# Optimization experiments

Measured on AMD Instinct MI355X. Metric: run time of the kernel, lower is better.

## Reference

```python
import jax, jax.numpy as jnp
import numpy as np
from jax import lax

N_GROUPS = 128
EPS = 1e-5


def _instance_norm(x):
    # x: [B, C, H, W]; per-sample per-channel normalization over spatial dims
    mean = jnp.mean(x, axis=(2, 3), keepdims=True)
    var = jnp.mean(jnp.square(x - mean), axis=(2, 3), keepdims=True)
    return (x - mean) * lax.rsqrt(var + EPS)


def _reflect_pad(x, p):
    return jnp.pad(x, ((0, 0), (0, 0), (p, p), (p, p)), mode='reflect')


def _conv(x, w, groups):
    # x: [N, Cin, H, W], w: [Cout, Cin/groups, kh, kw], VALID padding
    return lax.conv_general_dilated(
        x, w, window_strides=(1, 1), padding='VALID',
        dimension_numbers=('NCHW', 'OIHW', 'NCHW'),
        feature_group_count=groups)


def _forward_single(xi, ws, wp, b):
    # xi: [1, C, H, W]; ws: [C_mid, C/G, k, k]; wp: [C_pw, C_mid/G, 1, 1]; b: [C_pw]
    k = ws.shape[-1]
    p = (k - 1) // 2  # k=3 -> ceil/floor both 1
    y = _conv(_reflect_pad(xi, p), ws, N_GROUPS)
    y = _conv(y, wp, N_GROUPS) + b[None, :, None, None]
    return y


def setup_inputs() -> dict:
    key = jax.random.key(0)
    ks = jax.random.split(key, 6)
    B, C, H, W = 4, 512, 128, 128
    x = jax.random.normal(ks[0], (B, C, H, W), dtype=jnp.float32)
    w_spatial = jax.random.normal(ks[1], (B, 512, 4, 3, 3), dtype=jnp.float32) * 0.05
    w_pointwise = jax.random.normal(ks[2], (B, 128, 4, 1, 1), dtype=jnp.float32) * 0.05
    bias = jax.random.normal(ks[3], (B, 128), dtype=jnp.float32) * 0.05
    conv_w = jax.random.normal(ks[4], (512, 512, 3, 3), dtype=jnp.float32) * 0.02
    conv_b = jax.random.normal(ks[5], (512,), dtype=jnp.float32) * 0.02
    return {"x": x, "w_spatial": w_spatial, "w_pointwise": w_pointwise,
            "bias": bias, "conv_w": conv_w, "conv_b": conv_b}


def reference(x, w_spatial, w_pointwise, bias, conv_w, conv_b):
    B, C, H, W = x.shape
    x = _instance_norm(x)
    # per-sample grouped spatial + pointwise conv, vmapped over batch
    ys = jax.vmap(_forward_single)(x[:, None], w_spatial, w_pointwise, bias)
    # ys: [B, 1, C_pw, H, W] -> concat along channel dim as in torch.cat(dim=1)
    ys = ys.reshape(1, B * ys.shape[2], H, W)
    # final standard conv, reflect padding (1,1), kernel 3
    out = _conv(_reflect_pad(ys, 1), conv_w, 1) + conv_b[None, :, None, None]
    return out
```

## Files before the change

### kernel.cpp

```cpp
#include <hip/hip_runtime.h>
#include <hip/hip_bf16.h>


typedef unsigned short u16;
typedef __attribute__((ext_vector_type(8))) short bf16x8;
typedef __attribute__((ext_vector_type(4))) float f32x4;

#define HW 16384
#define NBC 2048

__device__ __forceinline__ int refl(int i) {
    return i < 0 ? -i : (i > 127 ? 254 - i : i);
}

__device__ __forceinline__ u16 f2bf(float f) {
    union { float f; unsigned u; } x; x.f = f;
    unsigned r = x.u + 0x7fffu + ((x.u >> 16) & 1u);
    return (u16)(r >> 16);
}

__device__ __forceinline__ void load_lds16(const u16* g, u16* l) {
    __builtin_amdgcn_global_load_lds(
        (const __attribute__((address_space(1))) unsigned int*)g,
        (__attribute__((address_space(3))) unsigned int*)l, 16, 0, 0);
}

__device__ __forceinline__ void load_lds16f(const float* g, float* l) {
    __builtin_amdgcn_global_load_lds(
        (const __attribute__((address_space(1))) unsigned int*)g,
        (__attribute__((address_space(3))) unsigned int*)l, 16, 0, 0);
}

__device__ __forceinline__ void load_lds4(const float* g, float* l) {
    __builtin_amdgcn_global_load_lds(
        (const __attribute__((address_space(1))) unsigned int*)g,
        (__attribute__((address_space(3))) unsigned int*)l, 4, 0, 0);
}

__global__ __launch_bounds__(256) void stats_kernel(
        const float* __restrict__ x, float* __restrict__ mean,
        float* __restrict__ rstd) {
    int bc = blockIdx.x;
    const float4* p4 = (const float4*)(x + (size_t)bc * HW);
    float s = 0.f, ss = 0.f;
    for (int i = threadIdx.x; i < HW / 4; i += 256) {
        float4 v = p4[i];
        s  += v.x + v.y + v.z + v.w;
        ss += v.x * v.x + v.y * v.y + v.z * v.z + v.w * v.w;
    }
    for (int o = 32; o >= 1; o >>= 1) {
        s  += __shfl_down(s, o);
        ss += __shfl_down(ss, o);
    }
    __shared__ float sm[4], sm2[4];
    int wid = threadIdx.x >> 6, lane = threadIdx.x & 63;
    if (lane == 0) { sm[wid] = s; sm2[wid] = ss; }
    __syncthreads();
    if (threadIdx.x == 0) {
        float S = sm[0] + sm[1] + sm[2] + sm[3];
        float SS = sm2[0] + sm2[1] + sm2[2] + sm2[3];
        float m = S * (1.f / HW);
        float var = SS * (1.f / HW) - m * m;
        mean[bc] = m;
        rstd[bc] = rsqrtf(var + 1e-5f);
    }
}

__global__ __launch_bounds__(256) void weff_kernel(
        const float* __restrict__ wsp, const float* __restrict__ wpw,
        const float* __restrict__ rstd, float* __restrict__ wf) {
    int idx = blockIdx.x * 256 + threadIdx.x;
    if (idx >= 4 * 128 * 4 * 9) return;
    int k = idx % 9;
    int c = (idx / 9) & 3;
    int g = (idx / 36) & 127;
    int b = idx / 4608;
    float acc = 0.f;
#pragma unroll
    for (int m = 0; m < 4; ++m) {
        acc += wpw[(b * 128 + g) * 4 + m] *
               wsp[(((size_t)b * 512 + g * 4 + m) * 4 + c) * 9 + k];
    }
    wf[idx] = acc * rstd[(b << 9) + (g << 2) + c];
}

__global__ __launch_bounds__(256) void bias_fold(
        const float* __restrict__ wf, const float* __restrict__ bias,
        const float* __restrict__ mean, float* __restrict__ bf) {
    int bg = blockIdx.x * 256 + threadIdx.x;
    if (bg >= 512) return;
    float s = bias[bg];
    const float* w = wf + bg * 36;
    const float* m = mean + (bg << 2);
#pragma unroll
    for (int j = 0; j < 36; ++j) s -= w[j] * m[j / 9];
    bf[bg] = s;
}

__global__ __launch_bounds__(256) void wpack_kernel(
        const float* __restrict__ cw, u16* __restrict__ wT) {
    __shared__ float s[4608];
    int t = threadIdx.x, co = blockIdx.x;
    const float* src = cw + (size_t)co * 4608;
    for (int i = t; i < 4608; i += 256) s[i] = src[i];
    __syncthreads();
#pragma unroll
    for (int tap = 0; tap < 9; ++tap) {
        u16* dst = &wT[((size_t)(tap << 9) + co) * 512];
        dst[t]       = f2bf(s[t * 9 + tap]);
        dst[t + 256] = f2bf(s[(t + 256) * 9 + tap]);
    }
}

__global__ __launch_bounds__(512) void midconv_fused(
        const float* __restrict__ x, const float* __restrict__ wf,
        const float* __restrict__ bf, u16* __restrict__ ysT) {
    __shared__ float mid[2][2560];
    __shared__ float halo[2][320];
    __shared__ u16 outb[128 * 72];
    __shared__ float s_w[4608];
    __shared__ float s_b[128];
    int t = threadIdx.x;
    int b = blockIdx.y;
    int x0 = (blockIdx.x & 7) << 4, y0 = (blockIdx.x >> 3) << 3;

    for (int i = t; i < 4608; i += 512) s_w[i] = wf[b * 4608 + i];
    if (t < 128) s_b[t] = bf[(b << 7) + t];

    int smid0, smid1, shalo;
    {
        int ch = t / 40, rem = t - ch * 40;
        int r = rem >> 2, j = rem & 3;
        smid0 = (ch << 14) + (refl(y0 + r - 1) << 7) + x0 + (j << 2);
        int i1 = t + 512 < 640 ? t + 512 : 0;
        ch = i1 / 40; rem = i1 - ch * 40; r = rem >> 2; j = rem & 3;
        smid1 = (ch << 14) + (refl(y0 + r - 1) << 7) + x0 + (j << 2);
        int ih = t < 320 ? t : 0;
        int side = ih >= 160;
        int hh = side ? ih - 160 : ih;
        ch = hh / 10; r = hh - ch * 10;
        int col = side ? refl(x0 + 16) : refl(x0 - 1);
        shalo = (ch << 14) + (refl(y0 + r - 1) << 7) + col;
    }

    int gq = t >> 7;
    int rem = t & 127;
    int py = rem >> 4, px = rem & 15;

    {
        const float* xq = x + ((size_t)(b << 9) << 14);
        load_lds16f(xq + smid0, &mid[0][t * 4]);
        if (t < 128) load_lds16f(xq + smid1, &mid[0][(512 + t) * 4]);
        if (t < 320) load_lds4(xq + shalo, &halo[0][t]);
    }

    for (int q = 0; q < 32; ++q) {
        __syncthreads();
        if (q == 16) {
            for (int i = t; i < 1024; i += 512) {
                int pix = i >> 3, seg = i & 7;
                bf16x8 v = *(const bf16x8*)&outb[pix * 72 + (seg << 3)];
                int ppy = pix >> 4, ppx = pix & 15;
                size_t gp = (size_t)(((y0 + ppy) << 7) + x0 + ppx);
                *(bf16x8*)&ysT[gp * 512 + (b << 7) + (seg << 3)] = v;
            }
            __syncthreads();
        }
        int cur = q & 1;
        if (q < 31) {
            const float* xq = x + ((size_t)((b << 9) + ((q + 1) << 4)) << 14);
            load_lds16f(xq + smid0, &mid[cur ^ 1][t * 4]);
            if (t < 128) load_lds16f(xq + smid1, &mid[cur ^ 1][(512 + t) * 4]);
            if (t < 320) load_lds4(xq + shalo, &halo[cur ^ 1][t]);
        }
        int group = (q << 2) + gq;
        float acc = s_b[group];
        const float* wq = &s_w[group * 36];
#pragma unroll
        for (int c = 0; c < 4; ++c) {
            const float* tp  = &mid[cur][(gq * 4 + c) * 160];
            const float* hlc = &halo[cur][(gq * 4 + c) * 10];
            const float* hrc = &halo[cur][160 + (gq * 4 + c) * 10];
#pragma unroll
            for (int kh = 0; kh < 3; ++kh) {
                int row = py + kh;
                const float* rp = tp + row * 16;
                float m0 = (px == 0)  ? hlc[row] : rp[px - 1];
                float m1 = rp[px];
                float m2 = (px == 15) ? hrc[row] : rp[px + 1];
                acc += wq[c * 9 + kh * 3 + 0] * m0 +
                       wq[c * 9 + kh * 3 + 1] * m1 +
                       wq[c * 9 + kh * 3 + 2] * m2;
            }
        }
        outb[(py * 16 + px) * 72 + (group & 63)] = f2bf(acc);
    }
    __syncthreads();
    for (int i = t; i < 1024; i += 512) {
        int pix = i >> 3, seg = i & 7;
        bf16x8 v = *(const bf16x8*)&outb[pix * 72 + (seg << 3)];
        int ppy = pix >> 4, ppx = pix & 15;
        size_t gp = (size_t)(((y0 + ppy) << 7) + x0 + ppx);
        *(bf16x8*)&ysT[gp * 512 + (b << 7) + 64 + (seg << 3)] = v;
    }
}

__global__ __launch_bounds__(256, 2) void finalconv_mfma(
        const u16* __restrict__ ysT, const u16* __restrict__ wT,
        const float* __restrict__ cb, float* __restrict__ out) {
    __shared__ u16 lds_ys[528 * 32];
    __shared__ u16 lds_wt[576 * 32];
    int t = threadIdx.x;
    int w = t >> 6, l = t & 63;
    int m = l & 15, q = l >> 4;
    int bid = blockIdx.x;
    int swz = ((bid & 7) << 6) + (bid >> 3);
    int co0 = (swz & 7) << 6;
    int y0 = (swz >> 3) << 1;
    int tr = w >> 1, xw = (w & 1) * 64;

    int ago_ys[9], ago_wt[9];
#pragma unroll
    for (int k = 0; k < 9; ++k) {
        int i = w + 4 * k;
        int i2 = i < 33 ? i : 0;
        int s = i2 * 64 + l;
        int p = s >> 2, c = s & 3;
        int pc = p > 519 ? 519 : p;
        int hr = (pc * 1009) >> 17;
        int hc = pc - hr * 130;
        int gy = refl(y0 + hr - 1), gx = refl(hc - 1);
        ago_ys[k] = ((gy << 7) + gx) * 512 + (c ^ ((p >> 1) & 3)) * 8;

        int s2 = i * 64 + l;
        int row = s2 >> 2, c2 = s2 & 3;
        int tap = row >> 6, co_l = row & 63;
        ago_wt[k] = ((tap << 9) + co0 + co_l) * 512 + (c2 ^ ((co_l >> 1) & 3)) * 8;
    }

    const u16* ap[4];
#pragma unroll
    for (int i = 0; i < 4; ++i) {
        int co_l = i * 16 + m;
        ap[i] = &lds_wt[co_l * 32 + (q ^ ((co_l >> 1) & 3)) * 8];
    }
    int P[4];
#pragma unroll
    for (int j = 0; j < 4; ++j) P[j] = tr * 130 + xw + j * 16 + m;

    f32x4 acc[4][4];
#pragma unroll
    for (int i = 0; i < 4; ++i)
#pragma unroll
        for (int j = 0; j < 4; ++j) acc[i][j] = (f32x4){0.f, 0.f, 0.f, 0.f};

    for (int ci0 = 0; ci0 < 512; ci0 += 32) {
        __syncthreads();
#pragma unroll
        for (int k = 0; k < 8; ++k)
            load_lds16(ysT + ago_ys[k] + ci0, &lds_ys[(w + 4 * k) * 512]);
        if (w == 0)
            load_lds16(ysT + ago_ys[8] + ci0, &lds_ys[32 * 512]);
#pragma unroll
        for (int k = 0; k < 9; ++k)
            load_lds16(wT + ago_wt[k] + ci0, &lds_wt[(w + 4 * k) * 512]);
        __syncthreads();
#pragma unroll
        for (int tap = 0; tap < 9; ++tap) {
            const int dyi = tap / 3, dxi = tap % 3;
            bf16x8 a[4], b[4];
#pragma unroll
            for (int i = 0; i < 4; ++i)
                a[i] = *(const bf16x8*)(ap[i] + tap * 2048);
#pragma unroll
            for (int j = 0; j < 4; ++j) {
                int p = P[j] + dyi * 130 + dxi;
                b[j] = *(const bf16x8*)&lds_ys[(p << 5) + ((q ^ ((p >> 1) & 3)) << 3)];
            }
#pragma unroll
            for (int i = 0; i < 4; ++i)
#pragma unroll
                for (int j = 0; j < 4; ++j)
                    acc[i][j] = __builtin_amdgcn_mfma_f32_16x16x32_bf16(
                        a[i], b[j], acc[i][j], 0, 0, 0);
        }
    }
    int gyo = y0 + tr;
#pragma unroll
    for (int i = 0; i < 4; ++i) {
        int cob = co0 + i * 16 + q * 4;
#pragma unroll
        for (int j = 0; j < 4; ++j) {
            int xx = xw + j * 16 + m;
            float* o = out + (size_t)cob * HW + (gyo << 7) + xx;
#pragma unroll
            for (int r = 0; r < 4; ++r)
                o[(size_t)r * HW] = acc[i][j][r] + cb[cob + r];
        }
    }
}

extern "C" void kernel_launch(void* const* d_in, const int* in_sizes, int n_in,
                              void* d_out, int out_size, void* d_ws, size_t ws_size,
                              hipStream_t stream) {
    const float* x    = (const float*)d_in[0];
    const float* wsp  = (const float*)d_in[1];
    const float* wpw  = (const float*)d_in[2];
    const float* bias = (const float*)d_in[3];
    const float* cw   = (const float*)d_in[4];
    const float* cb   = (const float*)d_in[5];
    float* out = (float*)d_out;

    char* ws = (char*)d_ws;
    u16*   ysT  = (u16*)ws;
    u16*   wT   = (u16*)(ws + 16777216);
    float* mean = (float*)(ws + 21495808);
    float* rstd = (float*)(ws + 21504000);
    float* wf   = (float*)(ws + 21512192);
    float* bf   = (float*)(ws + 21585920);

    stats_kernel<<<NBC, 256, 0, stream>>>(x, mean, rstd);
    weff_kernel<<<(4 * 128 * 4 * 9 + 255) / 256, 256, 0, stream>>>(wsp, wpw, rstd, wf);
    bias_fold<<<2, 256, 0, stream>>>(wf, bias, mean, bf);
    wpack_kernel<<<512, 256, 0, stream>>>(cw, wT);
    midconv_fused<<<dim3(128, 4), 512, 0, stream>>>(x, wf, bf, ysT);
    finalconv_mfma<<<512, 256, 0, stream>>>(ysT, wT, cb, out);
}
```

Measured before the change: 356.3 us.

## Split midconv channel groups across grid z, fuse weight and bias folding kernels

The midconv grid gains a dimension that splits the 128 groups per sample into four quarters of 32. Each block now loops 8 times instead of 32 and loads only its slice of folded weights and bias. This raises the block count fourfold to improve occupancy and shorten the serial chain per block, and shrinks LDS use. The output buffer becomes float with a stride of 33 to avoid bank conflicts, with bf16 conversion moved to the final store. Separately, the weight-fold and bias-fold kernels are merged into one kernel using a wavefront reduction, saving a launch. The cost is halo re-reads and setup repeated per block.

```diff
diff --git a/kernel.cpp b/kernel.cpp
--- a/kernel.cpp
+++ b/kernel.cpp
@@ -66,35 +66,28 @@
     }
 }
 
-__global__ __launch_bounds__(256) void weff_kernel(
+__global__ __launch_bounds__(64) void weff_bias_kernel(
         const float* __restrict__ wsp, const float* __restrict__ wpw,
-        const float* __restrict__ rstd, float* __restrict__ wf) {
-    int idx = blockIdx.x * 256 + threadIdx.x;
-    if (idx >= 4 * 128 * 4 * 9) return;
-    int k = idx % 9;
-    int c = (idx / 9) & 3;
-    int g = (idx / 36) & 127;
-    int b = idx / 4608;
-    float acc = 0.f;
-#pragma unroll
-    for (int m = 0; m < 4; ++m) {
-        acc += wpw[(b * 128 + g) * 4 + m] *
-               wsp[(((size_t)b * 512 + g * 4 + m) * 4 + c) * 9 + k];
-    }
-    wf[idx] = acc * rstd[(b << 9) + (g << 2) + c];
-}
-
-__global__ __launch_bounds__(256) void bias_fold(
-        const float* __restrict__ wf, const float* __restrict__ bias,
-        const float* __restrict__ mean, float* __restrict__ bf) {
-    int bg = blockIdx.x * 256 + threadIdx.x;
-    if (bg >= 512) return;
-    float s = bias[bg];
-    const float* w = wf + bg * 36;
-    const float* m = mean + (bg << 2);
-#pragma unroll
-    for (int j = 0; j < 36; ++j) s -= w[j] * m[j / 9];
-    bf[bg] = s;
+        const float* __restrict__ rstd, const float* __restrict__ mean,
+        const float* __restrict__ bias, float* __restrict__ wf,
+        float* __restrict__ bf) {
+    int bg = blockIdx.x;
+    int b = bg >> 7, g = bg & 127;
+    int t = threadIdx.x;
+    float contrib = 0.f;
+    if (t < 36) {
+        int c = t / 9, k = t - c * 9;
+        float acc = 0.f;
+#pragma unroll
+        for (int m = 0; m < 4; ++m)
+            acc += wpw[bg * 4 + m] *
+                   wsp[(((size_t)(b << 9) + (g << 2) + m) * 4 + c) * 9 + k];
+        float v = acc * rstd[(b << 9) + (g << 2) + c];
+        wf[bg * 36 + t] = v;
+        contrib = v * mean[(b << 9) + (g << 2) + c];
+    }
+    for (int o = 32; o >= 1; o >>= 1) contrib += __shfl_down(contrib, o);
+    if (t == 0) bf[bg] = bias[bg] - contrib;
 }
 
 __global__ __launch_bounds__(256) void wpack_kernel(
@@ -117,15 +110,16 @@
         const float* __restrict__ bf, u16* __restrict__ ysT) {
     __shared__ float mid[2][2560];
     __shared__ float halo[2][320];
-    __shared__ u16 outb[128 * 72];
-    __shared__ float s_w[4608];
-    __shared__ float s_b[128];
+    __shared__ float outb[128 * 33];
+    __shared__ float s_w[1152];
+    __shared__ float s_b[32];
     int t = threadIdx.x;
-    int b = blockIdx.y;
+    int qr = blockIdx.y;
+    int b = blockIdx.z;
     int x0 = (blockIdx.x & 7) << 4, y0 = (blockIdx.x >> 3) << 3;
 
-    for (int i = t; i < 4608; i += 512) s_w[i] = wf[b * 4608 + i];
-    if (t < 128) s_b[t] = bf[(b << 7) + t];
+    for (int i = t; i < 1152; i += 512) s_w[i] = wf[b * 4608 + qr * 1152 + i];
+    if (t < 32) s_b[t] = bf[(b << 7) + (qr << 5) + t];
 
     int smid0, smid1, shalo;
     {
@@ -146,36 +140,27 @@
     int gq = t >> 7;
     int rem = t & 127;
     int py = rem >> 4, px = rem & 15;
+    int ch_base = (b << 9) + (qr << 7);
 
     {
-        const float* xq = x + ((size_t)(b << 9) << 14);
+        const float* xq = x + ((size_t)ch_base << 14);
         load_lds16f(xq + smid0, &mid[0][t * 4]);
         if (t < 128) load_lds16f(xq + smid1, &mid[0][(512 + t) * 4]);
         if (t < 320) load_lds4(xq + shalo, &halo[0][t]);
     }
 
-    for (int q = 0; q < 32; ++q) {
+    for (int q = 0; q < 8; ++q) {
         __syncthreads();
-        if (q == 16) {
-            for (int i = t; i < 1024; i += 512) {
-                int pix = i >> 3, seg = i & 7;
-                bf16x8 v = *(const bf16x8*)&outb[pix * 72 + (seg << 3)];
-                int ppy = pix >> 4, ppx = pix & 15;
-                size_t gp = (size_t)(((y0 + ppy) << 7) + x0 + ppx);
-                *(bf16x8*)&ysT[gp * 512 + (b << 7) + (seg << 3)] = v;
-            }
-            __syncthreads();
-        }
         int cur = q & 1;
-        if (q < 31) {
-            const float* xq = x + ((size_t)((b << 9) + ((q + 1) << 4)) << 14);
+        if (q < 7) {
+            const float* xq = x + ((size_t)(ch_base + ((q + 1) << 4)) << 14);
             load_lds16f(xq + smid0, &mid[cur ^ 1][t * 4]);
             if (t < 128) load_lds16f(xq + smid1, &mid[cur ^ 1][(512 + t) * 4]);
             if (t < 320) load_lds4(xq + shalo, &halo[cur ^ 1][t]);
         }
-        int group = (q << 2) + gq;
-        float acc = s_b[group];
-        const float* wq = &s_w[group * 36];
+        int col = (q << 2) + gq;
+        float acc = s_b[col];
+        const float* wq = &s_w[col * 36];
 #pragma unroll
         for (int c = 0; c < 4; ++c) {
             const float* tp  = &mid[cur][(gq * 4 + c) * 160];
@@ -193,15 +178,18 @@
                        wq[c * 9 + kh * 3 + 2] * m2;
             }
         }
-        outb[(py * 16 + px) * 72 + (group & 63)] = f2bf(acc);
+        outb[(py * 16 + px) * 33 + col] = acc;
     }
     __syncthreads();
-    for (int i = t; i < 1024; i += 512) {
-        int pix = i >> 3, seg = i & 7;
-        bf16x8 v = *(const bf16x8*)&outb[pix * 72 + (seg << 3)];
+    {
+        int pix = t >> 2, seg = t & 3;
+        const float* src = &outb[pix * 33 + (seg << 3)];
+        bf16x8 v;
+#pragma unroll
+        for (int j = 0; j < 8; ++j) v[j] = (short)f2bf(src[j]);
         int ppy = pix >> 4, ppx = pix & 15;
         size_t gp = (size_t)(((y0 + ppy) << 7) + x0 + ppx);
-        *(bf16x8*)&ysT[gp * 512 + (b << 7) + 64 + (seg << 3)] = v;
+        *(bf16x8*)&ysT[gp * 512 + (b << 7) + (qr << 5) + (seg << 3)] = v;
     }
 }
 
@@ -320,9 +308,8 @@
     float* bf   = (float*)(ws + 21585920);
 
     stats_kernel<<<NBC, 256, 0, stream>>>(x, mean, rstd);
-    weff_kernel<<<(4 * 128 * 4 * 9 + 255) / 256, 256, 0, stream>>>(wsp, wpw, rstd, wf);
-    bias_fold<<<2, 256, 0, stream>>>(wf, bias, mean, bf);
+    weff_bias_kernel<<<512, 64, 0, stream>>>(wsp, wpw, rstd, mean, bias, wf, bf);
     wpack_kernel<<<512, 256, 0, stream>>>(cw, wT);
-    midconv_fused<<<dim3(128, 4), 512, 0, stream>>>(x, wf, bf, ysT);
+    midconv_fused<<<dim3(128, 4, 4), 512, 0, stream>>>(x, wf, bf, ysT);
     finalconv_mfma<<<512, 256, 0, stream>>>(ysT, wT, cb, out);
 }
```

After: 355.5 us. No clear change (-0.2%).
